# Performance work log

Measured on AMD Instinct MI355X. Metric: run time of the kernel, lower is better.

The kernel has to match this reference:

```python
import jax, jax.numpy as jnp
import numpy as np

B = 1
N_HEADS = 8
SEQ = 4096
HEAD_DIM = 128
BLOCK = 64          # sparse_block_size == kernel_block_size
LOCAL_BLOCKS = 16
VERT_STRIDE = 8


def _token_mask():
    """Local + vertical-strided block-sparse causal mask, per head.

    Block (qb, kb) is active for head h iff qb >= kb and
    (qb - kb < LOCAL_BLOCKS  or  (kb + h*head_step + 1) % VERT_STRIDE == 0),
    then expanded to token level and AND-ed with the token causal mask.
    """
    nb = SEQ // BLOCK
    qb = jnp.arange(nb)[:, None]                      # [nb, 1]
    kb = jnp.arange(nb)[None, :]                      # [1, nb]
    head_step = max(1, VERT_STRIDE // N_HEADS)        # hetero heads (homo_head=False)
    h = jnp.arange(N_HEADS)[:, None, None]            # [H, 1, 1]
    vert = (kb[None] + h * head_step + 1) % VERT_STRIDE == 0   # [H, 1, nb] -> broadcast
    local = (qb - kb >= 0) & (qb - kb < LOCAL_BLOCKS)          # [nb, nb]
    bmask = (qb >= kb)[None] & (local[None] | vert)            # [H, nb, nb]
    # expand block mask to token level
    tmask = jnp.repeat(jnp.repeat(bmask, BLOCK, axis=1), BLOCK, axis=2)  # [H, S, S]
    causal = jnp.arange(SEQ)[:, None] >= jnp.arange(SEQ)[None, :]
    return tmask & causal[None]


def setup_inputs() -> dict:
    key = jax.random.key(0)
    kq, kk, kv = jax.random.split(key, 3)
    q = jax.random.normal(kq, (B, N_HEADS, SEQ, HEAD_DIM), jnp.float32)
    k = jax.random.normal(kk, (B, N_HEADS, SEQ, HEAD_DIM), jnp.float32)
    v = jax.random.normal(kv, (B, N_HEADS, SEQ, HEAD_DIM), jnp.float32)
    sm_scale = jnp.float32(1.0 / np.sqrt(HEAD_DIM))
    return {"q": q, "k": k, "v": v, "sm_scale": sm_scale}


def reference(q, k, v, sm_scale):
    mask = _token_mask()                                       # [H, S, S] bool
    scores = jnp.einsum('bhqd,bhkd->bhqk', q, k) * sm_scale    # [B, H, S, S]
    neg = jnp.asarray(jnp.finfo(scores.dtype).min, scores.dtype)
    scores = jnp.where(mask[None], scores, neg)
    p = jax.nn.softmax(scores, axis=-1)
    return jnp.einsum('bhqk,bhkd->bhqd', p, v)
```

## Files before the change

kernel.cpp:

```cpp
#include <hip/hip_runtime.h>
#include <hip/hip_bf16.h>

#define HH 8
#define SEQL 4096
#define DD 128
#define NBLK 64
#define LOCAL_B 16
#define MBIAS 12.0f
#define EP_STR 132

typedef __attribute__((ext_vector_type(8))) short bf16x8;
typedef __attribute__((ext_vector_type(4))) float f32x4;
typedef unsigned short ushort_t;

typedef const __attribute__((address_space(1))) unsigned int gu32;
typedef __attribute__((address_space(3))) unsigned int lu32;

__device__ __forceinline__ unsigned short f2bf(float x) {
    union { float f; unsigned u; } a; a.f = x;
    unsigned r = a.u + 0x7FFFu + ((a.u >> 16) & 1u);
    return (unsigned short)(r >> 16);
}

__device__ __forceinline__ unsigned cvtpk_bf16(float lo, float hi) {
    unsigned r;
    asm("v_cvt_pk_bf16_f32 %0, %1, %2" : "=v"(r) : "v"(lo), "v"(hi));
    return r;
}

__device__ __forceinline__ void gload16(const void* src, void* ldsdst) {
    __builtin_amdgcn_global_load_lds((gu32*)src, (lu32*)ldsdst, 16, 0, 0);
}

#define T_STR 136
__global__ void prep(const float* __restrict__ k, const float* __restrict__ v,
                     ushort_t* __restrict__ kb, ushort_t* __restrict__ vt) {
    __shared__ ushort_t t[64 * T_STR];
    int bid = blockIdx.x;
    int tid = threadIdx.x;
    if (bid < 2048) {
        int idx = (bid * 256 + tid) * 8;
        const float4* s = (const float4*)(k + idx);
        float4 a = s[0], b = s[1];
        union { bf16x8 v8; ushort_t u[8]; } p;
        p.u[0] = f2bf(a.x); p.u[1] = f2bf(a.y); p.u[2] = f2bf(a.z); p.u[3] = f2bf(a.w);
        p.u[4] = f2bf(b.x); p.u[5] = f2bf(b.y); p.u[6] = f2bf(b.z); p.u[7] = f2bf(b.w);
        *(bf16x8*)(kb + idx) = p.v8;
        return;
    }
    int g = bid - 2048;
    int h  = g >> 6;
    int sb = g & 63;
    const float* vp = v + ((size_t)h * SEQL + sb * 64) * DD;
    {
        int col = (tid & 15) * 8;
        #pragma unroll
        for (int it = 0; it < 4; ++it) {
            int row = it * 16 + (tid >> 4);
            const float4* s = (const float4*)(vp + row * DD + col);
            float4 a = s[0], b = s[1];
            union { bf16x8 v8; ushort_t u[8]; } p;
            p.u[0] = f2bf(a.x); p.u[1] = f2bf(a.y); p.u[2] = f2bf(a.z); p.u[3] = f2bf(a.w);
            p.u[4] = f2bf(b.x); p.u[5] = f2bf(b.y); p.u[6] = f2bf(b.z); p.u[7] = f2bf(b.w);
            *(bf16x8*)&t[row * T_STR + col] = p.v8;
        }
    }
    __syncthreads();
    {
        int d = tid >> 1, seg = tid & 1;
        ushort_t* dst = vt + ((size_t)h * DD + d) * SEQL + sb * 64 + seg * 32;
        #pragma unroll
        for (int i = 0; i < 4; ++i) {
            union { bf16x8 v8; ushort_t u[8]; } o;
            #pragma unroll
            for (int e = 0; e < 8; ++e)
                o.u[e] = t[(seg * 32 + i * 8 + e) * T_STR + d];
            *(bf16x8*)(dst + i * 8) = o.v8;
        }
    }
}

__global__ __launch_bounds__(128, 4)
void bsattn7(const float* __restrict__ q, const ushort_t* __restrict__ kbuf,
             const ushort_t* __restrict__ vtbuf, const float* __restrict__ scl,
             float* __restrict__ out) {
    const int g = blockIdx.x;
    const int h = g & 7;
    const int u = g >> 3;
    const int qb   = (u < 64) ? (63 - (u >> 1)) : (31 - ((u - 64) >> 1));
    const int half = u & 1;
    const int tid = threadIdx.x;
    const int w  = tid >> 6;
    const int l  = tid & 63;
    const int lr = l & 15;
    const int lg = l >> 4;

    __shared__ char smem[32768];

    const float kappa = scl[0] * 1.44269504088896f;

    const float*    qh = q     + (size_t)h * SEQL * DD;
    const ushort_t* kh = kbuf  + (size_t)h * SEQL * DD;
    const ushort_t* vh = vtbuf + (size_t)h * DD * SEQL;
    float*          oh = out   + (size_t)h * SEQL * DD;

    bf16x8 qf[4];
    {
        const float* qrow = qh + (size_t)(qb * 64 + half * 32 + 16 * w + lr) * DD;
        #pragma unroll
        for (int ks = 0; ks < 4; ++ks) {
            const float4* p4 = (const float4*)(qrow + ks * 32 + lg * 8);
            float4 x = p4[0], y = p4[1];
            union { bf16x8 v8; ushort_t u[8]; } pk;
            pk.u[0] = f2bf(x.x * kappa); pk.u[1] = f2bf(x.y * kappa);
            pk.u[2] = f2bf(x.z * kappa); pk.u[3] = f2bf(x.w * kappa);
            pk.u[4] = f2bf(y.x * kappa); pk.u[5] = f2bf(y.y * kappa);
            pk.u[6] = f2bf(y.z * kappa); pk.u[7] = f2bf(y.w * kappa);
            qf[ks] = pk.v8;
        }
    }

    f32x4 oacc[8];
    #pragma unroll
    for (int i = 0; i < 8; ++i) oacc[i] = (f32x4){0.f, 0.f, 0.f, 0.f};
    float lrun = 0.f;

    unsigned kA = (unsigned)(lr * 256) + (unsigned)((lg * 16) ^ ((lr & 7) << 4));
    unsigned kB = kA ^ 64u;
    unsigned vA = 16384u + (unsigned)(lr * 64) + (unsigned)((lg * 16) ^ ((lr & 3) << 4));
    unsigned kst = 0, vst = 0;

    auto stage = [&](int s) {
        const char* kbase = (const char*)kh + (size_t)s * 8192;
        #pragma unroll
        for (int i = 0; i < 4; ++i) {
            int a = i * 2048 + w * 1024 + l * 16;
            int row = a >> 8, cl = a & 255;
            gload16(kbase + row * 256 + (cl ^ ((row & 7) << 4)),
                    smem + kst + i * 2048 + w * 1024);
        }
        const char* vbase = (const char*)vh + (size_t)s * 64;
        #pragma unroll
        for (int i = 0; i < 4; ++i) {
            int a = i * 2048 + w * 1024 + l * 16;
            int d = a >> 6, cl = a & 63;
            gload16(vbase + (size_t)d * (SEQL * 2) + (cl ^ ((d & 3) << 4)),
                    smem + 16384 + vst + i * 2048 + w * 1024);
        }
        kst ^= 8192u; vst ^= 8192u;
    };

    const bool selA = (lg >= 2);
    const bool b1 = (lg & 1);
    const bool b2 = (lg & 2);

    auto compute = [&](bool diag) {
        f32x4 sacc[2];
        #pragma unroll
        for (int ct = 0; ct < 2; ++ct)
            sacc[ct] = (f32x4){-MBIAS, -MBIAS, -MBIAS, -MBIAS};
        __builtin_amdgcn_s_setprio(1);
        #pragma unroll
        for (int ks = 0; ks < 4; ++ks) {
            #pragma unroll
            for (int ct = 0; ct < 2; ++ct) {
                bf16x8 kf = *(const bf16x8*)(smem + ((ks & 1) ? kB : kA) +
                                             ct * 4096 + (ks >> 1) * 128);
                sacc[ct] = __builtin_amdgcn_mfma_f32_16x16x32_bf16(kf, qf[ks], sacc[ct], 0, 0, 0);
            }
        }
        __builtin_amdgcn_s_setprio(0);

        float p[2][4];
        #pragma unroll
        for (int ct = 0; ct < 2; ++ct)
            #pragma unroll
            for (int j = 0; j < 4; ++j)
                p[ct][j] = exp2f(sacc[ct][j]);
        if (diag) {
            #pragma unroll
            for (int ct = 0; ct < 2; ++ct)
                #pragma unroll
                for (int j = 0; j < 4; ++j)
                    if (16 * ct + 4 * lg + j > 16 * w + lr) p[ct][j] = 0.f;
        }
        float rs = 0.f;
        #pragma unroll
        for (int ct = 0; ct < 2; ++ct)
            #pragma unroll
            for (int j = 0; j < 4; ++j) rs += p[ct][j];
        lrun += rs;

        unsigned e0 = cvtpk_bf16(p[0][0], p[0][1]), e1 = cvtpk_bf16(p[0][2], p[0][3]);
        unsigned o0 = cvtpk_bf16(p[1][0], p[1][1]), o1 = cvtpk_bf16(p[1][2], p[1][3]);

        union { unsigned u[4]; bf16x8 v8; } pb0;
        {
            unsigned m = selA ? o0 : e0, nn = selA ? e0 : o0;
            unsigned t  = __shfl_xor((int)nn, 32);
            unsigned tp = __shfl_xor((int)nn, 48);
            unsigned m16 = __shfl_xor((int)m, 16);
            pb0.u[0] = b1 ? (b2 ? m16 : tp) : (b2 ? t : m);
            pb0.u[2] = b1 ? (b2 ? m : t) : (b2 ? tp : m16);
        }
        {
            unsigned m = selA ? o1 : e1, nn = selA ? e1 : o1;
            unsigned t  = __shfl_xor((int)nn, 32);
            unsigned tp = __shfl_xor((int)nn, 48);
            unsigned m16 = __shfl_xor((int)m, 16);
            pb0.u[1] = b1 ? (b2 ? m16 : tp) : (b2 ? t : m);
            pb0.u[3] = b1 ? (b2 ? m : t) : (b2 ? tp : m16);
        }

        __builtin_amdgcn_s_setprio(1);
        #pragma unroll
        for (int dt = 0; dt < 8; ++dt) {
            bf16x8 vf = *(const bf16x8*)(smem + vA + dt * 1024);
            oacc[dt] = __builtin_amdgcn_mfma_f32_16x16x32_bf16(vf, pb0.v8, oacc[dt], 0, 0, 0);
        }
        __builtin_amdgcn_s_setprio(0);
    };

    const int vstart = (7 - h) & 7;
    const int lo = (qb >= 15) ? (qb - 15) : 0;
    int kb = (vstart <= qb - LOCAL_B) ? vstart : lo;
    int ph = 0;
    stage(kb * 2);
    for (;;) {
        const bool masked = (kb == qb) && (!half || ph == 1);
        bool last;
        int nkb = kb, nph = 0;
        if (ph == 0) {
            if (kb == qb && half == 0) last = true;
            else { nph = 1; last = false; }
        } else {
            if (kb == qb) last = true;
            else {
                nkb = (kb < lo) ? ((kb + 8 <= qb - LOCAL_B) ? kb + 8 : lo) : (kb + 1);
                last = false;
            }
        }

        if (!last) {
            stage(nkb * 2 + nph);
            asm volatile("s_waitcnt vmcnt(8)" ::: "memory");
        } else {
            asm volatile("s_waitcnt vmcnt(0)" ::: "memory");
        }
        __builtin_amdgcn_sched_barrier(0);
        __builtin_amdgcn_s_barrier();
        __builtin_amdgcn_sched_barrier(0);
        compute(masked);
        __builtin_amdgcn_s_barrier();
        kA ^= 8192u; kB ^= 8192u; vA ^= 8192u;
        if (last) break;
        kb = nkb; ph = nph;
    }

    float tot = lrun;
    tot += __shfl_xor(tot, 16);
    tot += __shfl_xor(tot, 32);
    float rcp = 1.0f / tot;

    float* ep  = (float*)smem;
    float* epw = ep + w * 16 * EP_STR;
    #pragma unroll
    for (int dt = 0; dt < 8; ++dt)
        #pragma unroll
        for (int j = 0; j < 4; ++j)
            epw[lr * EP_STR + dt * 16 + 4 * lg + j] = oacc[dt][j] * rcp;
    __syncthreads();
    {
        int qr  = tid >> 2;
        int seg = tid & 3;
        const float* rp = ep + (qr >> 4) * (16 * EP_STR) + (qr & 15) * EP_STR + seg * 32;
        float* op = oh + (size_t)(qb * 64 + half * 32 + qr) * DD + seg * 32;
        #pragma unroll
        for (int i = 0; i < 8; ++i)
            ((float4*)op)[i] = ((const float4*)rp)[i];
    }
}

extern "C" void kernel_launch(void* const* d_in, const int* in_sizes, int n_in,
                              void* d_out, int out_size, void* d_ws, size_t ws_size,
                              hipStream_t stream) {
    const float* q   = (const float*)d_in[0];
    const float* k   = (const float*)d_in[1];
    const float* v   = (const float*)d_in[2];
    const float* scl = (const float*)d_in[3];
    float* out = (float*)d_out;

    ushort_t* Kb = (ushort_t*)d_ws;
    ushort_t* Vt = Kb + (size_t)HH * SEQL * DD;

    prep<<<dim3(2048 + HH * 64), dim3(256), 0, stream>>>(k, v, Kb, Vt);
    bsattn7<<<dim3(HH * 128), dim3(128), 0, stream>>>(q, Kb, Vt, scl, out);
}
```

Before: 69.97 us.

## Use 512-thread blocks per full query block with split-K key halves

Each workgroup now covers a full 64-row query block using 8 waves: 4 waves over query rows times 2 key-column groups that each take 32 of the 64 keys per tile. Full 64-key tiles are staged per iteration instead of two 32-key phases, which halves loop iterations and removes the half-block scheduling logic. The two key-group partial outputs and row sums are merged through shared memory in the epilogue. It doubles LDS use to 64KB and cuts the grid to 512 blocks, which may reduce occupancy and adds a cross-wave reduction.

```diff
diff --git a/kernel.cpp b/kernel.cpp
--- a/kernel.cpp
+++ b/kernel.cpp
@@ -80,22 +80,23 @@
     }
 }
 
-__global__ __launch_bounds__(128, 4)
-void bsattn7(const float* __restrict__ q, const ushort_t* __restrict__ kbuf,
+__global__ __launch_bounds__(512, 4)
+void bsattn8(const float* __restrict__ q, const ushort_t* __restrict__ kbuf,
              const ushort_t* __restrict__ vtbuf, const float* __restrict__ scl,
              float* __restrict__ out) {
-    const int g = blockIdx.x;
-    const int h = g & 7;
-    const int u = g >> 3;
-    const int qb   = (u < 64) ? (63 - (u >> 1)) : (31 - ((u - 64) >> 1));
-    const int half = u & 1;
+    const int g  = blockIdx.x;
+    const int h  = g & 7;
+    const int i0 = g >> 3;
+    const int qb = (i0 < 32) ? (63 - i0) : (i0 - 32);
     const int tid = threadIdx.x;
     const int w  = tid >> 6;
+    const int wq = w & 3;
+    const int kg = w >> 2;
     const int l  = tid & 63;
     const int lr = l & 15;
     const int lg = l >> 4;
 
-    __shared__ char smem[32768];
+    __shared__ char smem[65536];
 
     const float kappa = scl[0] * 1.44269504088896f;
 
@@ -106,7 +107,7 @@
 
     bf16x8 qf[4];
     {
-        const float* qrow = qh + (size_t)(qb * 64 + half * 32 + 16 * w + lr) * DD;
+        const float* qrow = qh + (size_t)(qb * 64 + 16 * wq + lr) * DD;
         #pragma unroll
         for (int ks = 0; ks < 4; ++ks) {
             const float4* p4 = (const float4*)(qrow + ks * 32 + lg * 8);
@@ -125,29 +126,29 @@
     for (int i = 0; i < 8; ++i) oacc[i] = (f32x4){0.f, 0.f, 0.f, 0.f};
     float lrun = 0.f;
 
-    unsigned kA = (unsigned)(lr * 256) + (unsigned)((lg * 16) ^ ((lr & 7) << 4));
+    unsigned kA = (unsigned)(kg * 8192 + lr * 256) + (unsigned)((lg * 16) ^ ((lr & 7) << 4));
     unsigned kB = kA ^ 64u;
-    unsigned vA = 16384u + (unsigned)(lr * 64) + (unsigned)((lg * 16) ^ ((lr & 3) << 4));
+    unsigned vA = 32768u + (unsigned)(lr * 128) + (unsigned)(((kg * 64) + lg * 16) ^ ((lr & 7) << 4));
     unsigned kst = 0, vst = 0;
 
-    auto stage = [&](int s) {
-        const char* kbase = (const char*)kh + (size_t)s * 8192;
-        #pragma unroll
-        for (int i = 0; i < 4; ++i) {
-            int a = i * 2048 + w * 1024 + l * 16;
-            int row = a >> 8, cl = a & 255;
-            gload16(kbase + row * 256 + (cl ^ ((row & 7) << 4)),
-                    smem + kst + i * 2048 + w * 1024);
-        }
-        const char* vbase = (const char*)vh + (size_t)s * 64;
-        #pragma unroll
-        for (int i = 0; i < 4; ++i) {
-            int a = i * 2048 + w * 1024 + l * 16;
-            int d = a >> 6, cl = a & 63;
-            gload16(vbase + (size_t)d * (SEQL * 2) + (cl ^ ((d & 3) << 4)),
-                    smem + 16384 + vst + i * 2048 + w * 1024);
-        }
-        kst ^= 8192u; vst ^= 8192u;
+    auto stage = [&](int kb) {
+        const char* kbase = (const char*)(kh + (size_t)kb * 64 * DD);
+        #pragma unroll
+        for (int j = 0; j < 2; ++j) {
+            int row = j * 32 + w * 4 + (l >> 4);
+            int col = (l & 15) * 16;
+            gload16(kbase + row * 256 + (col ^ ((row & 7) << 4)),
+                    smem + kst + j * 8192 + w * 1024);
+        }
+        const char* vbase = (const char*)vh + (size_t)kb * 128;
+        #pragma unroll
+        for (int j = 0; j < 2; ++j) {
+            int d = j * 64 + w * 8 + (l >> 3);
+            int col = (l & 7) * 16;
+            gload16(vbase + (size_t)d * (SEQL * 2) + (col ^ ((d & 7) << 4)),
+                    smem + 32768 + vst + j * 8192 + w * 1024);
+        }
+        kst ^= 16384u; vst ^= 16384u;
     };
 
     const bool selA = (lg >= 2);
@@ -182,7 +183,7 @@
             for (int ct = 0; ct < 2; ++ct)
                 #pragma unroll
                 for (int j = 0; j < 4; ++j)
-                    if (16 * ct + 4 * lg + j > 16 * w + lr) p[ct][j] = 0.f;
+                    if (kg * 32 + ct * 16 + 4 * lg + j > 16 * wq + lr) p[ct][j] = 0.f;
         }
         float rs = 0.f;
         #pragma unroll
@@ -194,89 +195,93 @@
         unsigned e0 = cvtpk_bf16(p[0][0], p[0][1]), e1 = cvtpk_bf16(p[0][2], p[0][3]);
         unsigned o0 = cvtpk_bf16(p[1][0], p[1][1]), o1 = cvtpk_bf16(p[1][2], p[1][3]);
 
-        union { unsigned u[4]; bf16x8 v8; } pb0;
+        union { unsigned u[4]; bf16x8 v8; } pb;
         {
             unsigned m = selA ? o0 : e0, nn = selA ? e0 : o0;
             unsigned t  = __shfl_xor((int)nn, 32);
             unsigned tp = __shfl_xor((int)nn, 48);
             unsigned m16 = __shfl_xor((int)m, 16);
-            pb0.u[0] = b1 ? (b2 ? m16 : tp) : (b2 ? t : m);
-            pb0.u[2] = b1 ? (b2 ? m : t) : (b2 ? tp : m16);
+            pb.u[0] = b1 ? (b2 ? m16 : tp) : (b2 ? t : m);
+            pb.u[2] = b1 ? (b2 ? m : t) : (b2 ? tp : m16);
         }
         {
             unsigned m = selA ? o1 : e1, nn = selA ? e1 : o1;
             unsigned t  = __shfl_xor((int)nn, 32);
             unsigned tp = __shfl_xor((int)nn, 48);
             unsigned m16 = __shfl_xor((int)m, 16);
-            pb0.u[1] = b1 ? (b2 ? m16 : tp) : (b2 ? t : m);
-            pb0.u[3] = b1 ? (b2 ? m : t) : (b2 ? tp : m16);
+            pb.u[1] = b1 ? (b2 ? m16 : tp) : (b2 ? t : m);
+            pb.u[3] = b1 ? (b2 ? m : t) : (b2 ? tp : m16);
         }
 
         __builtin_amdgcn_s_setprio(1);
         #pragma unroll
         for (int dt = 0; dt < 8; ++dt) {
-            bf16x8 vf = *(const bf16x8*)(smem + vA + dt * 1024);
-            oacc[dt] = __builtin_amdgcn_mfma_f32_16x16x32_bf16(vf, pb0.v8, oacc[dt], 0, 0, 0);
+            bf16x8 vf = *(const bf16x8*)(smem + vA + dt * 2048);
+            oacc[dt] = __builtin_amdgcn_mfma_f32_16x16x32_bf16(vf, pb.v8, oacc[dt], 0, 0, 0);
         }
         __builtin_amdgcn_s_setprio(0);
     };
 
     const int vstart = (7 - h) & 7;
-    const int lo = (qb >= 15) ? (qb - 15) : 0;
+    int lo = qb - (LOCAL_B - 1); if (lo < 0) lo = 0;
     int kb = (vstart <= qb - LOCAL_B) ? vstart : lo;
-    int ph = 0;
-    stage(kb * 2);
+    stage(kb);
     for (;;) {
-        const bool masked = (kb == qb) && (!half || ph == 1);
-        bool last;
-        int nkb = kb, nph = 0;
-        if (ph == 0) {
-            if (kb == qb && half == 0) last = true;
-            else { nph = 1; last = false; }
-        } else {
-            if (kb == qb) last = true;
-            else {
-                nkb = (kb < lo) ? ((kb + 8 <= qb - LOCAL_B) ? kb + 8 : lo) : (kb + 1);
-                last = false;
-            }
-        }
-
-        if (!last) {
-            stage(nkb * 2 + nph);
-            asm volatile("s_waitcnt vmcnt(8)" ::: "memory");
+        int kn;
+        if (kb < lo) { int n = kb + 8; kn = (n <= qb - LOCAL_B) ? n : lo; }
+        else if (kb < qb) kn = kb + 1;
+        else kn = -1;
+
+        if (kn >= 0) {
+            stage(kn);
+            asm volatile("s_waitcnt vmcnt(4)" ::: "memory");
         } else {
             asm volatile("s_waitcnt vmcnt(0)" ::: "memory");
         }
         __builtin_amdgcn_sched_barrier(0);
         __builtin_amdgcn_s_barrier();
         __builtin_amdgcn_sched_barrier(0);
-        compute(masked);
+        compute(kb == qb);
         __builtin_amdgcn_s_barrier();
-        kA ^= 8192u; kB ^= 8192u; vA ^= 8192u;
-        if (last) break;
-        kb = nkb; ph = nph;
+        kA ^= 16384u; kB ^= 16384u; vA ^= 16384u;
+        if (kn < 0) break;
+        kb = kn;
     }
 
     float tot = lrun;
     tot += __shfl_xor(tot, 16);
     tot += __shfl_xor(tot, 32);
-    float rcp = 1.0f / tot;
-
-    float* ep  = (float*)smem;
-    float* epw = ep + w * 16 * EP_STR;
-    #pragma unroll
-    for (int dt = 0; dt < 8; ++dt)
-        #pragma unroll
-        for (int j = 0; j < 4; ++j)
-            epw[lr * EP_STR + dt * 16 + 4 * lg + j] = oacc[dt][j] * rcp;
+
+    float* ep   = (float*)smem;
+    float* lsum = (float*)(smem + 33792);
+    float* epw  = ep + wq * 16 * EP_STR;
+    if (kg == 1) {
+        #pragma unroll
+        for (int dt = 0; dt < 8; ++dt)
+            #pragma unroll
+            for (int j = 0; j < 4; ++j)
+                epw[lr * EP_STR + dt * 16 + 4 * lg + j] = oacc[dt][j];
+        if (lg == 0) lsum[wq * 16 + lr] = tot;
+    }
+    __syncthreads();
+    if (kg == 0) {
+        float rcp = 1.0f / (tot + lsum[wq * 16 + lr]);
+        #pragma unroll
+        for (int dt = 0; dt < 8; ++dt)
+            #pragma unroll
+            for (int j = 0; j < 4; ++j) {
+                int ix = lr * EP_STR + dt * 16 + 4 * lg + j;
+                epw[ix] = (epw[ix] + oacc[dt][j]) * rcp;
+            }
+    }
     __syncthreads();
     {
-        int qr  = tid >> 2;
-        int seg = tid & 3;
-        const float* rp = ep + (qr >> 4) * (16 * EP_STR) + (qr & 15) * EP_STR + seg * 32;
-        float* op = oh + (size_t)(qb * 64 + half * 32 + qr) * DD + seg * 32;
-        #pragma unroll
-        for (int i = 0; i < 8; ++i)
+        int qr  = tid >> 3;
+        int seg = tid & 7;
+        const float* rp = ep + (qr >> 4) * (16 * EP_STR) + (qr & 15) * EP_STR + seg * 16;
+        float* op = oh + (size_t)(qb * 64 + qr) * DD + seg * 16;
+        #pragma unroll
+        for (int i = 0; i < 4; ++i)
             ((float4*)op)[i] = ((const float4*)rp)[i];
     }
 }
@@ -294,5 +299,5 @@
     ushort_t* Vt = Kb + (size_t)HH * SEQL * DD;
 
     prep<<<dim3(2048 + HH * 64), dim3(256), 0, stream>>>(k, v, Kb, Vt);
-    bsattn7<<<dim3(HH * 128), dim3(128), 0, stream>>>(q, Kb, Vt, scl, out);
-}
+    bsattn8<<<dim3(HH * NBLK), dim3(512), 0, stream>>>(q, Kb, Vt, scl, out);
+}
```

Result: faster. 57.25 us (-18.2%).
